# Kernel tuning notes

Measured on AMD Instinct MI355X. Metric: run time of the kernel, lower is better.

The kernel has to match this reference:

```python
import jax, jax.numpy as jnp
import numpy as np
import math

DIM = 1024
N_HEADS = 16
HEAD_DIM = DIM // N_HEADS


def rope(x):
    # x: [B, H, S, D] with D == HEAD_DIM, interleaved even/odd rotation
    S = x.shape[-2]
    D = x.shape[-1]
    pos = jnp.arange(S, dtype=x.dtype)[:, None]              # [S, 1]
    dim = jnp.arange(D // 2, dtype=x.dtype)[None, :]         # [1, D/2]
    theta = pos / jnp.exp(2.0 * dim / D * math.log(10000.0))  # [S, D/2]
    sin = jnp.sin(theta)[None, None]                          # [1,1,S,D/2]
    cos = jnp.cos(theta)[None, None]
    x1 = x[..., ::2]
    x2 = x[..., 1::2]
    out1 = x1 * cos - x2 * sin
    out2 = x1 * sin + x2 * cos
    # interleave back: stack on last axis then flatten pairs
    return jnp.stack([out1, out2], axis=-1).reshape(x.shape)


def setup_inputs() -> dict:
    key = jax.random.key(0)
    ks = jax.random.split(key, 9)
    B, S = 2, 2048
    s = 1.0 / math.sqrt(DIM)
    inp = {
        "x": jax.random.normal(ks[0], (B, S, DIM), dtype=jnp.float32),
        "wq": jax.random.normal(ks[1], (DIM, DIM), dtype=jnp.float32) * s,
        "bq": jnp.zeros((DIM,), dtype=jnp.float32),
        "wk": jax.random.normal(ks[2], (DIM, DIM), dtype=jnp.float32) * s,
        "bk": jnp.zeros((DIM,), dtype=jnp.float32),
        "wv": jax.random.normal(ks[3], (DIM, DIM), dtype=jnp.float32) * s,
        "bv": jnp.zeros((DIM,), dtype=jnp.float32),
        "wo": jax.random.normal(ks[4], (DIM, DIM), dtype=jnp.float32) * s,
        "bo": jnp.zeros((DIM,), dtype=jnp.float32),
    }
    return inp


def reference(x, wq, bq, wk, bk, wv, bv, wo, bo):
    B, S, _ = x.shape
    # torch Linear: y = x @ W^T + b
    def proj(w, b):
        y = jnp.einsum('bsd,ed->bse', x, w) + b
        return y.reshape(B, S, N_HEADS, HEAD_DIM).transpose(0, 2, 1, 3)  # [B,H,S,Dh]
    q = rope(proj(wq, bq))
    k = rope(proj(wk, bk))
    v = proj(wv, bv)
    score = jnp.einsum('bhqd,bhkd->bhqk', q, k) / math.sqrt(HEAD_DIM)
    causal = jnp.tril(jnp.ones((S, S), dtype=bool))
    score = jnp.where(causal[None, None], score, -jnp.inf)
    attn = jax.nn.softmax(score, axis=-1)
    out = jnp.einsum('bhqk,bhkd->bhqd', attn, v)
    out = out.transpose(0, 2, 1, 3).reshape(B, S, DIM)
    return jnp.einsum('bsd,ed->bse', out, wo) + bo
```

## Files before the change

### kernel.cpp

```cpp
#include <hip/hip_runtime.h>
#include <cstdint>
#include <cstddef>


typedef __bf16 bf16_t;
typedef __bf16 bf16x8 __attribute__((ext_vector_type(8)));
typedef __bf16 bf16x4 __attribute__((ext_vector_type(4)));
typedef float  f32x4  __attribute__((ext_vector_type(4)));

#define DEVFN __device__ __forceinline__

static constexpr int Bn  = 2;
static constexpr int S   = 2048;
static constexpr int DIM = 1024;
static constexpr int NH  = 16;
static constexpr int HD  = 64;
static constexpr int Mrows = Bn * S;

DEVFN f32x4 mfma16(bf16x8 a, bf16x8 b, f32x4 c) {
  return __builtin_amdgcn_mfma_f32_16x16x32_bf16(a, b, c, 0, 0, 0);
}

DEVFN void gl_lds16(const bf16_t* g, bf16_t* l) {
  __builtin_amdgcn_global_load_lds(
      (const __attribute__((address_space(1))) unsigned*)g,
      (__attribute__((address_space(3))) unsigned*)l, 16, 0, 0);
}

__global__ __launch_bounds__(256) void k_cvt(const float* __restrict__ in,
                                             bf16_t* __restrict__ out, int n) {
  int i = (blockIdx.x * 256 + threadIdx.x) * 4;
  if (i >= n) return;
  float4 v = *(const float4*)(in + i);
  bf16x4 o = { (bf16_t)v.x, (bf16_t)v.y, (bf16_t)v.z, (bf16_t)v.w };
  *(bf16x4*)(out + i) = o;
}

__global__ __launch_bounds__(256) void k_tab(float2* __restrict__ tab) {
  int i = blockIdx.x * 256 + threadIdx.x;
  int s = i >> 5, d = i & 31;
  float th = (float)s * expf(-(2.0f * (float)d / 64.0f) * logf(10000.0f));
  tab[i] = make_float2(cosf(th), sinf(th));
}

__global__ __launch_bounds__(256) void k_rope(bf16_t* __restrict__ X,
                                              const float2* __restrict__ tab,
                                              float scale) {
  int i = blockIdx.x * 256 + threadIdx.x;
  int row = i >> 7;
  int s = row & (S - 1);
  int dd = (i & 7) << 3;
  int p0 = dd >> 1;
  bf16x8 v = *(bf16x8*)(X + (size_t)i * 8);
  bf16x8 o;
#pragma unroll
  for (int j = 0; j < 4; ++j) {
    float x1 = (float)v[2 * j], x2 = (float)v[2 * j + 1];
    float2 cs = tab[s * 32 + p0 + j];
    o[2 * j]     = (bf16_t)((x1 * cs.x - x2 * cs.y) * scale);
    o[2 * j + 1] = (bf16_t)((x1 * cs.y + x2 * cs.x) * scale);
  }
  *(bf16x8*)(X + (size_t)i * 8) = o;
}

__global__ __launch_bounds__(256) void k_trans(const bf16_t* __restrict__ Vin,
                                               bf16_t* __restrict__ VT) {
  __shared__ __align__(16) bf16_t tile[64][72];
  int s0 = blockIdx.x * 64, bh = blockIdx.y;
  int b = bh >> 4, h = bh & 15;
  int t = threadIdx.x;
#pragma unroll
  for (int it = 0; it < 2; ++it) {
    int sl = (t >> 3) + it * 32, d0 = (t & 7) << 3;
    *(bf16x8*)&tile[sl][d0] =
        *(const bf16x8*)(Vin + (size_t)(b * S + s0 + sl) * DIM + h * HD + d0);
  }
  __syncthreads();
  int d = t >> 2, c0 = (t & 3) * 16;
  bf16_t buf[16];
#pragma unroll
  for (int j = 0; j < 16; ++j) buf[j] = tile[c0 + j][d];
  bf16_t* op = VT + ((size_t)bh * HD + d) * S + s0 + c0;
  *(bf16x8*)op = *(bf16x8*)&buf[0];
  *(bf16x8*)(op + 8) = *(bf16x8*)&buf[8];
}

template <bool OUTF32>
__global__ __launch_bounds__(256) void k_gemm(
    const bf16_t* __restrict__ A,
    const bf16_t* __restrict__ B0, const bf16_t* __restrict__ B1,
    const bf16_t* __restrict__ B2,
    const float* __restrict__ c0, const float* __restrict__ c1,
    const float* __restrict__ c2,
    void* O0, void* O1, void* O2, int Mg, int Ng, int Kg) {
  const bf16_t* Bw = blockIdx.z == 0 ? B0 : (blockIdx.z == 1 ? B1 : B2);
  const float* bias = blockIdx.z == 0 ? c0 : (blockIdx.z == 1 ? c1 : c2);
  void* Ov = blockIdx.z == 0 ? O0 : (blockIdx.z == 1 ? O1 : O2);

  __shared__ __align__(16) bf16_t Al[128 * 32];
  __shared__ __align__(16) bf16_t Bl[128 * 32];
  const int t = threadIdx.x, w = t >> 6, l = t & 63;
  const int lr = l & 15, lc = l >> 4;
  const int m0 = blockIdx.y * 128, n0 = blockIdx.x * 128;
  const int wr = w >> 1, wc = w & 1;
  f32x4 acc[4][4] = {};

  for (int k0 = 0; k0 < Kg; k0 += 32) {
    __syncthreads();
#pragma unroll
    for (int ld = 0; ld < 2; ++ld) {
      int c = t + ld * 256;
      int row = c >> 2, j = (c & 3) << 3;
      bf16_t* dstA = Al + (size_t)(w * 64 + ld * 256) * 8;
      bf16_t* dstB = Bl + (size_t)(w * 64 + ld * 256) * 8;
      gl_lds16(A + (size_t)(m0 + row) * Kg + k0 + j, dstA);
      gl_lds16(Bw + (size_t)(n0 + row) * Kg + k0 + j, dstB);
    }
    __syncthreads();
    bf16x8 af[4], bfr[4];
#pragma unroll
    for (int mi = 0; mi < 4; ++mi)
      af[mi] = *(const bf16x8*)(Al + (wr * 64 + mi * 16 + lr) * 32 + lc * 8);
#pragma unroll
    for (int ni = 0; ni < 4; ++ni)
      bfr[ni] = *(const bf16x8*)(Bl + (wc * 64 + ni * 16 + lr) * 32 + lc * 8);
#pragma unroll
    for (int mi = 0; mi < 4; ++mi)
#pragma unroll
      for (int ni = 0; ni < 4; ++ni)
        acc[mi][ni] = mfma16(af[mi], bfr[ni], acc[mi][ni]);
  }

#pragma unroll
  for (int ni = 0; ni < 4; ++ni) {
    int col = n0 + wc * 64 + ni * 16 + lr;
    float bv = bias[col];
#pragma unroll
    for (int mi = 0; mi < 4; ++mi) {
#pragma unroll
      for (int r = 0; r < 4; ++r) {
        int row = m0 + wr * 64 + mi * 16 + lc * 4 + r;
        float v = acc[mi][ni][r] + bv;
        if (OUTF32)
          ((float*)Ov)[(size_t)row * Ng + col] = v;
        else
          ((bf16_t*)Ov)[(size_t)row * Ng + col] = (bf16_t)v;
      }
    }
  }
}

DEVFN void stage_kv(const bf16_t* __restrict__ Kc,
                    const bf16_t* __restrict__ VT, bf16_t* Kb, bf16_t* Vb,
                    int b, int bh, int h, int k0, int t, int w) {
#pragma unroll
  for (int ld = 0; ld < 2; ++ld) {
    int c = t + ld * 256;
    int row = c >> 3;
    int j = ((c & 7) ^ (row & 7)) << 3;
    bf16_t* dstK = Kb + (size_t)(w * 64 + ld * 256) * 8;
    bf16_t* dstV = Vb + (size_t)(w * 64 + ld * 256) * 8;
    gl_lds16(Kc + (size_t)(b * S + k0 + row) * DIM + h * HD + j, dstK);
    gl_lds16(VT + ((size_t)bh * HD + row) * S + k0 + j, dstV);
  }
}

__global__ __launch_bounds__(256) void k_attn(const bf16_t* __restrict__ Q,
                                              const bf16_t* __restrict__ Kc,
                                              const bf16_t* __restrict__ VT,
                                              bf16_t* __restrict__ O) {
  __shared__ __align__(16) bf16_t Kl[2][64 * 64];
  __shared__ __align__(16) bf16_t Vl[2][64 * 64];
  __shared__ __align__(16) bf16_t Pl[4][16 * 64];
  const int t = threadIdx.x, w = t >> 6, l = t & 63;
  const int lr = l & 15, lc = l >> 4;
  const int lid = blockIdx.x + (blockIdx.y << 4);
  const int xcd = lid & 7, slot = lid >> 3;
  const int bh = xcd * 4 + (slot >> 4);
  const int a = slot & 15;
  const int b = bh >> 4, h = bh & 15;
  char* Pw = (char*)&Pl[w][0];

#pragma unroll 1
  for (int pi = 0; pi < 2; ++pi) {
    const int tile = (pi == 0) ? a : 31 - a;
    const int q0 = tile * 64;
    const int nt = tile + 1;

    bf16x8 qf[2];
    {
      const bf16_t* qp =
          Q + (size_t)(b * S + q0 + w * 16 + lr) * DIM + h * HD + lc * 8;
      qf[0] = *(const bf16x8*)qp;
      qf[1] = *(const bf16x8*)(qp + 32);
    }
    f32x4 o[4] = {};
    float m_run = -INFINITY;
    float rowsum = 0.f;

    stage_kv(Kc, VT, &Kl[0][0], &Vl[0][0], b, bh, h, 0, t, w);
    asm volatile("s_waitcnt vmcnt(0)" ::: "memory");
    __builtin_amdgcn_s_barrier();
    __builtin_amdgcn_sched_barrier(0);

#pragma unroll 1
    for (int it = 0; it < nt; ++it) {
      const int cur = it & 1;
      const bf16_t* Kb = &Kl[cur][0];
      const bf16_t* Vb = &Vl[cur][0];
      if (it + 1 < nt) {
        stage_kv(Kc, VT, &Kl[cur ^ 1][0], &Vl[cur ^ 1][0], b, bh, h,
                 (it + 1) * 64, t, w);
        asm volatile("s_waitcnt vmcnt(4)" ::: "memory");
      } else {
        asm volatile("s_waitcnt vmcnt(0)" ::: "memory");
      }
      __builtin_amdgcn_s_barrier();
      __builtin_amdgcn_sched_barrier(0);

      f32x4 s[4] = {};
      __builtin_amdgcn_s_setprio(1);
#pragma unroll
      for (int ks = 0; ks < 2; ++ks) {
#pragma unroll
        for (int ni = 0; ni < 4; ++ni) {
          int row = ni * 16 + lr;
          int off = (ks * 64 + lc * 16) ^ ((row & 7) << 4);
          bf16x8 kf = *(const bf16x8*)((const char*)Kb + row * 128 + off);
          s[ni] = mfma16(kf, qf[ks], s[ni]);
        }
      }
      __builtin_amdgcn_s_setprio(0);

      if (it == tile) {
        const int qloc = w * 16 + lr;
#pragma unroll
        for (int ni = 0; ni < 4; ++ni)
#pragma unroll
          for (int r = 0; r < 4; ++r)
            if (ni * 16 + lc * 4 + r > qloc) s[ni][r] = -INFINITY;
      }

      float pm = s[0][0];
#pragma unroll
      for (int ni = 0; ni < 4; ++ni)
#pragma unroll
        for (int r = 0; r < 4; ++r) pm = fmaxf(pm, s[ni][r]);
      pm = fmaxf(pm, __shfl_xor(pm, 16));
      pm = fmaxf(pm, __shfl_xor(pm, 32));

      if (__ballot(pm > m_run + 8.f)) {
        float mn = fmaxf(m_run, pm);
        float alpha = __expf(m_run - mn);
        m_run = mn;
        rowsum *= alpha;
#pragma unroll
        for (int r = 0; r < 4; ++r) {
          float aq = __shfl(alpha, lc * 4 + r);
#pragma unroll
          for (int ni = 0; ni < 4; ++ni) o[ni][r] *= aq;
        }
      }

      float rs = 0.f;
#pragma unroll
      for (int ni = 0; ni < 4; ++ni) {
        float p0 = __expf(s[ni][0] - m_run);
        float p1 = __expf(s[ni][1] - m_run);
        float p2 = __expf(s[ni][2] - m_run);
        float p3 = __expf(s[ni][3] - m_run);
        rs += (p0 + p1) + (p2 + p3);
        bf16x4 pb = { (bf16_t)p0, (bf16_t)p1, (bf16_t)p2, (bf16_t)p3 };
        *(bf16x4*)(Pw + (lr * 128 + ((ni * 32 + lc * 8) ^ ((lr & 7) << 4)))) =
            pb;
      }
      rs += __shfl_xor(rs, 16);
      rs += __shfl_xor(rs, 32);
      rowsum += rs;

      __builtin_amdgcn_s_setprio(1);
#pragma unroll
      for (int ks = 0; ks < 2; ++ks) {
        int off = ks * 64 + lc * 16;
        bf16x8 pa =
            *(const bf16x8*)(Pw + lr * 128 + (off ^ ((lr & 7) << 4)));
#pragma unroll
        for (int ni = 0; ni < 4; ++ni) {
          int vrow = ni * 16 + lr;
          bf16x8 vb = *(const bf16x8*)((const char*)Vb + vrow * 128 +
                                       (off ^ ((vrow & 7) << 4)));
          o[ni] = mfma16(pa, vb, o[ni]);
        }
      }
      __builtin_amdgcn_s_setprio(0);

      __builtin_amdgcn_s_barrier();
    }

    float inv[4];
#pragma unroll
    for (int r = 0; r < 4; ++r) inv[r] = 1.0f / __shfl(rowsum, lc * 4 + r);
#pragma unroll
    for (int ni = 0; ni < 4; ++ni)
#pragma unroll
      for (int r = 0; r < 4; ++r) {
        int qr = q0 + w * 16 + lc * 4 + r;
        float v = o[ni][r] * inv[r];
        O[(size_t)(b * S + qr) * DIM + h * HD + ni * 16 + lr] = (bf16_t)v;
      }
  }
}

extern "C" void kernel_launch(void* const* d_in, const int* in_sizes, int n_in,
                              void* d_out, int out_size, void* d_ws,
                              size_t ws_size, hipStream_t stream) {
  const float* x  = (const float*)d_in[0];
  const float* wq = (const float*)d_in[1];
  const float* bq = (const float*)d_in[2];
  const float* wk = (const float*)d_in[3];
  const float* bk = (const float*)d_in[4];
  const float* wv = (const float*)d_in[5];
  const float* bv = (const float*)d_in[6];
  const float* wo = (const float*)d_in[7];
  const float* bo = (const float*)d_in[8];

  const size_t MD = (size_t)Mrows * DIM;
  const size_t WD = (size_t)DIM * DIM;
  bf16_t* W = (bf16_t*)d_ws;
  bf16_t* x_bf  = W;
  bf16_t* wq_bf = x_bf + MD;
  bf16_t* wk_bf = wq_bf + WD;
  bf16_t* wv_bf = wk_bf + WD;
  bf16_t* wo_bf = wv_bf + WD;
  bf16_t* q_lin = wo_bf + WD;
  bf16_t* k_lin = q_lin + MD;
  bf16_t* v_lin = k_lin + MD;
  bf16_t* vT    = v_lin + MD;
  float2* tab   = (float2*)(vT + MD);
  bf16_t* attn_out = v_lin;

  k_cvt<<<4096, 256, 0, stream>>>(x, x_bf, (int)MD);
  k_cvt<<<1024, 256, 0, stream>>>(wq, wq_bf, (int)WD);
  k_cvt<<<1024, 256, 0, stream>>>(wk, wk_bf, (int)WD);
  k_cvt<<<1024, 256, 0, stream>>>(wv, wv_bf, (int)WD);
  k_cvt<<<1024, 256, 0, stream>>>(wo, wo_bf, (int)WD);
  k_tab<<<256, 256, 0, stream>>>(tab);

  k_gemm<false><<<dim3(DIM / 128, Mrows / 128, 3), 256, 0, stream>>>(
      x_bf, wq_bf, wk_bf, wv_bf, bq, bk, bv, q_lin, k_lin, v_lin, Mrows, DIM,
      DIM);

  k_rope<<<2048, 256, 0, stream>>>(q_lin, tab, 0.125f);
  k_rope<<<2048, 256, 0, stream>>>(k_lin, tab, 1.0f);
  k_trans<<<dim3(S / 64, Bn * NH), 256, 0, stream>>>(v_lin, vT);

  k_attn<<<dim3(16, Bn * NH), 256, 0, stream>>>(q_lin, k_lin, vT, attn_out);

  k_gemm<true><<<dim3(DIM / 128, Mrows / 128, 1), 256, 0, stream>>>(
      attn_out, wo_bf, wo_bf, wo_bf, bo, bo, bo, d_out, d_out, d_out, Mrows,
      DIM, DIM);
}
```

Before: 143.1 us.

## Fuse prep kernels, fold RoPE and V transpose into QKV GEMM, pipeline attention

The six conversion and table kernels are merged into a single prep launch. RoPE (with the query scale) and the V transpose are moved into the QKV GEMM epilogue, which removes three separate passes over Q, K and V in global memory. The attention loop is software-pipelined: QK^T for the next tile is computed before the softmax of the current one, and V uses a triple buffer. The costs are a scattered transposed-store epilogue for V, extra shuffles and table reads in the RoPE epilogue, and higher register and LDS use in attention.

```diff
diff --git a/kernel.cpp b/kernel.cpp
--- a/kernel.cpp
+++ b/kernel.cpp
@@ -27,75 +27,48 @@
       (__attribute__((address_space(3))) unsigned*)l, 16, 0, 0);
 }
 
-__global__ __launch_bounds__(256) void k_cvt(const float* __restrict__ in,
-                                             bf16_t* __restrict__ out, int n) {
-  int i = (blockIdx.x * 256 + threadIdx.x) * 4;
-  if (i >= n) return;
-  float4 v = *(const float4*)(in + i);
-  bf16x4 o = { (bf16_t)v.x, (bf16_t)v.y, (bf16_t)v.z, (bf16_t)v.w };
-  *(bf16x4*)(out + i) = o;
-}
-
-__global__ __launch_bounds__(256) void k_tab(float2* __restrict__ tab) {
-  int i = blockIdx.x * 256 + threadIdx.x;
-  int s = i >> 5, d = i & 31;
-  float th = (float)s * expf(-(2.0f * (float)d / 64.0f) * logf(10000.0f));
-  tab[i] = make_float2(cosf(th), sinf(th));
-}
-
-__global__ __launch_bounds__(256) void k_rope(bf16_t* __restrict__ X,
-                                              const float2* __restrict__ tab,
-                                              float scale) {
-  int i = blockIdx.x * 256 + threadIdx.x;
-  int row = i >> 7;
-  int s = row & (S - 1);
-  int dd = (i & 7) << 3;
-  int p0 = dd >> 1;
-  bf16x8 v = *(bf16x8*)(X + (size_t)i * 8);
-  bf16x8 o;
-#pragma unroll
-  for (int j = 0; j < 4; ++j) {
-    float x1 = (float)v[2 * j], x2 = (float)v[2 * j + 1];
-    float2 cs = tab[s * 32 + p0 + j];
-    o[2 * j]     = (bf16_t)((x1 * cs.x - x2 * cs.y) * scale);
-    o[2 * j + 1] = (bf16_t)((x1 * cs.y + x2 * cs.x) * scale);
-  }
-  *(bf16x8*)(X + (size_t)i * 8) = o;
-}
-
-__global__ __launch_bounds__(256) void k_trans(const bf16_t* __restrict__ Vin,
-                                               bf16_t* __restrict__ VT) {
-  __shared__ __align__(16) bf16_t tile[64][72];
-  int s0 = blockIdx.x * 64, bh = blockIdx.y;
-  int b = bh >> 4, h = bh & 15;
-  int t = threadIdx.x;
-#pragma unroll
-  for (int it = 0; it < 2; ++it) {
-    int sl = (t >> 3) + it * 32, d0 = (t & 7) << 3;
-    *(bf16x8*)&tile[sl][d0] =
-        *(const bf16x8*)(Vin + (size_t)(b * S + s0 + sl) * DIM + h * HD + d0);
-  }
-  __syncthreads();
-  int d = t >> 2, c0 = (t & 3) * 16;
-  bf16_t buf[16];
-#pragma unroll
-  for (int j = 0; j < 16; ++j) buf[j] = tile[c0 + j][d];
-  bf16_t* op = VT + ((size_t)bh * HD + d) * S + s0 + c0;
-  *(bf16x8*)op = *(bf16x8*)&buf[0];
-  *(bf16x8*)(op + 8) = *(bf16x8*)&buf[8];
-}
-
-template <bool OUTF32>
-__global__ __launch_bounds__(256) void k_gemm(
-    const bf16_t* __restrict__ A,
-    const bf16_t* __restrict__ B0, const bf16_t* __restrict__ B1,
-    const bf16_t* __restrict__ B2,
+__global__ __launch_bounds__(256) void k_prep(
+    const float* __restrict__ x, const float* __restrict__ wq,
+    const float* __restrict__ wk, const float* __restrict__ wv,
+    const float* __restrict__ wo, bf16_t* __restrict__ xb,
+    bf16_t* __restrict__ wqb, bf16_t* __restrict__ wkb,
+    bf16_t* __restrict__ wvb, bf16_t* __restrict__ wob,
+    float2* __restrict__ tab) {
+  const int bid = blockIdx.x;
+  if (bid < 8192) {
+    const float* src;
+    bf16_t* dst;
+    size_t base;
+    if (bid < 4096) {
+      src = x; dst = xb; base = (size_t)bid << 10;
+    } else {
+      int wsel = (bid - 4096) >> 10;
+      src = wsel == 0 ? wq : wsel == 1 ? wk : wsel == 2 ? wv : wo;
+      dst = wsel == 0 ? wqb : wsel == 1 ? wkb : wsel == 2 ? wvb : wob;
+      base = (size_t)((bid - 4096) & 1023) << 10;
+    }
+    size_t i = base + (size_t)threadIdx.x * 4;
+    float4 v = *(const float4*)(src + i);
+    bf16x4 o = { (bf16_t)v.x, (bf16_t)v.y, (bf16_t)v.z, (bf16_t)v.w };
+    *(bf16x4*)(dst + i) = o;
+  } else {
+    int i = (bid - 8192) * 256 + threadIdx.x;
+    int s = i >> 5, d = i & 31;
+    float th = (float)s * expf((float)d * -0.2878231366f);
+    tab[i] = make_float2(cosf(th), sinf(th));
+  }
+}
+
+__global__ __launch_bounds__(256) void k_gemm_qkv(
+    const bf16_t* __restrict__ A, const bf16_t* __restrict__ B0,
+    const bf16_t* __restrict__ B1, const bf16_t* __restrict__ B2,
     const float* __restrict__ c0, const float* __restrict__ c1,
-    const float* __restrict__ c2,
-    void* O0, void* O1, void* O2, int Mg, int Ng, int Kg) {
-  const bf16_t* Bw = blockIdx.z == 0 ? B0 : (blockIdx.z == 1 ? B1 : B2);
-  const float* bias = blockIdx.z == 0 ? c0 : (blockIdx.z == 1 ? c1 : c2);
-  void* Ov = blockIdx.z == 0 ? O0 : (blockIdx.z == 1 ? O1 : O2);
+    const float* __restrict__ c2, bf16_t* __restrict__ Oq,
+    bf16_t* __restrict__ Ok, bf16_t* __restrict__ VTo,
+    const float2* __restrict__ tab) {
+  const int z = blockIdx.z;
+  const bf16_t* Bw = z == 0 ? B0 : (z == 1 ? B1 : B2);
+  const float* bias = z == 0 ? c0 : (z == 1 ? c1 : c2);
 
   __shared__ __align__(16) bf16_t Al[128 * 32];
   __shared__ __align__(16) bf16_t Bl[128 * 32];
@@ -105,7 +78,7 @@
   const int wr = w >> 1, wc = w & 1;
   f32x4 acc[4][4] = {};
 
-  for (int k0 = 0; k0 < Kg; k0 += 32) {
+  for (int k0 = 0; k0 < DIM; k0 += 32) {
     __syncthreads();
 #pragma unroll
     for (int ld = 0; ld < 2; ++ld) {
@@ -113,8 +86,87 @@
       int row = c >> 2, j = (c & 3) << 3;
       bf16_t* dstA = Al + (size_t)(w * 64 + ld * 256) * 8;
       bf16_t* dstB = Bl + (size_t)(w * 64 + ld * 256) * 8;
-      gl_lds16(A + (size_t)(m0 + row) * Kg + k0 + j, dstA);
-      gl_lds16(Bw + (size_t)(n0 + row) * Kg + k0 + j, dstB);
+      gl_lds16(A + (size_t)(m0 + row) * DIM + k0 + j, dstA);
+      gl_lds16(Bw + (size_t)(n0 + row) * DIM + k0 + j, dstB);
+    }
+    __syncthreads();
+    bf16x8 af[4], bfr[4];
+#pragma unroll
+    for (int mi = 0; mi < 4; ++mi)
+      af[mi] = *(const bf16x8*)(Al + (wr * 64 + mi * 16 + lr) * 32 + lc * 8);
+#pragma unroll
+    for (int ni = 0; ni < 4; ++ni)
+      bfr[ni] = *(const bf16x8*)(Bl + (wc * 64 + ni * 16 + lr) * 32 + lc * 8);
+#pragma unroll
+    for (int mi = 0; mi < 4; ++mi)
+#pragma unroll
+      for (int ni = 0; ni < 4; ++ni)
+        acc[mi][ni] = mfma16(af[mi], bfr[ni], acc[mi][ni]);
+  }
+
+  if (z == 2) {
+    const int h = (n0 >> 6) + wc;
+#pragma unroll
+    for (int ni = 0; ni < 4; ++ni) {
+      const int d = ni * 16 + lr;
+      const float bv = bias[n0 + wc * 64 + ni * 16 + lr];
+#pragma unroll
+      for (int mi = 0; mi < 4; ++mi) {
+        int rowb = m0 + wr * 64 + mi * 16 + lc * 4;
+        int bb = rowb >> 11, ss = rowb & (S - 1);
+        bf16x4 pb = { (bf16_t)(acc[mi][ni][0] + bv),
+                      (bf16_t)(acc[mi][ni][1] + bv),
+                      (bf16_t)(acc[mi][ni][2] + bv),
+                      (bf16_t)(acc[mi][ni][3] + bv) };
+        *(bf16x4*)(VTo + ((size_t)(bb * NH + h) * HD + d) * S + ss) = pb;
+      }
+    }
+  } else {
+    bf16_t* Ov = z == 0 ? Oq : Ok;
+    const float scale = z == 0 ? 0.125f : 1.0f;
+#pragma unroll
+    for (int ni = 0; ni < 4; ++ni) {
+      const int col = n0 + wc * 64 + ni * 16 + lr;
+      const float bv = bias[col];
+      const int p0 = ni * 8 + (lr >> 1);
+#pragma unroll
+      for (int mi = 0; mi < 4; ++mi) {
+#pragma unroll
+        for (int r = 0; r < 4; ++r) {
+          int row = m0 + wr * 64 + mi * 16 + lc * 4 + r;
+          float v = acc[mi][ni][r] + bv;
+          float pt = __shfl_xor(v, 1);
+          float2 cs = tab[(row & (S - 1)) * 32 + p0];
+          float out = (lr & 1) ? (pt * cs.y + v * cs.x)
+                               : (v * cs.x - pt * cs.y);
+          Ov[(size_t)row * DIM + col] = (bf16_t)(out * scale);
+        }
+      }
+    }
+  }
+}
+
+__global__ __launch_bounds__(256) void k_gemm_out(
+    const bf16_t* __restrict__ A, const bf16_t* __restrict__ Bw,
+    const float* __restrict__ bias, float* __restrict__ Ov) {
+  __shared__ __align__(16) bf16_t Al[128 * 32];
+  __shared__ __align__(16) bf16_t Bl[128 * 32];
+  const int t = threadIdx.x, w = t >> 6, l = t & 63;
+  const int lr = l & 15, lc = l >> 4;
+  const int m0 = blockIdx.y * 128, n0 = blockIdx.x * 128;
+  const int wr = w >> 1, wc = w & 1;
+  f32x4 acc[4][4] = {};
+
+  for (int k0 = 0; k0 < DIM; k0 += 32) {
+    __syncthreads();
+#pragma unroll
+    for (int ld = 0; ld < 2; ++ld) {
+      int c = t + ld * 256;
+      int row = c >> 2, j = (c & 3) << 3;
+      bf16_t* dstA = Al + (size_t)(w * 64 + ld * 256) * 8;
+      bf16_t* dstB = Bl + (size_t)(w * 64 + ld * 256) * 8;
+      gl_lds16(A + (size_t)(m0 + row) * DIM + k0 + j, dstA);
+      gl_lds16(Bw + (size_t)(n0 + row) * DIM + k0 + j, dstB);
     }
     __syncthreads();
     bf16x8 af[4], bfr[4];
@@ -136,26 +188,21 @@
     int col = n0 + wc * 64 + ni * 16 + lr;
     float bv = bias[col];
 #pragma unroll
-    for (int mi = 0; mi < 4; ++mi) {
+    for (int mi = 0; mi < 4; ++mi)
 #pragma unroll
       for (int r = 0; r < 4; ++r) {
         int row = m0 + wr * 64 + mi * 16 + lc * 4 + r;
-        float v = acc[mi][ni][r] + bv;
-        if (OUTF32)
-          ((float*)Ov)[(size_t)row * Ng + col] = v;
-        else
-          ((bf16_t*)Ov)[(size_t)row * Ng + col] = (bf16_t)v;
-      }
-    }
+        Ov[(size_t)row * DIM + col] = acc[mi][ni][r] + bv;
+      }
   }
 }
 
 DEVFN void stage_kv(const bf16_t* __restrict__ Kc,
                     const bf16_t* __restrict__ VT, bf16_t* Kb, bf16_t* Vb,
-                    int b, int bh, int h, int k0, int t, int w) {
+                    int b, int bh, int h, int k0, int tid, int w) {
 #pragma unroll
   for (int ld = 0; ld < 2; ++ld) {
-    int c = t + ld * 256;
+    int c = tid + ld * 256;
     int row = c >> 3;
     int j = ((c & 7) ^ (row & 7)) << 3;
     bf16_t* dstK = Kb + (size_t)(w * 64 + ld * 256) * 8;
@@ -170,9 +217,9 @@
                                               const bf16_t* __restrict__ VT,
                                               bf16_t* __restrict__ O) {
   __shared__ __align__(16) bf16_t Kl[2][64 * 64];
-  __shared__ __align__(16) bf16_t Vl[2][64 * 64];
+  __shared__ __align__(16) bf16_t Vl[3][64 * 64];
   __shared__ __align__(16) bf16_t Pl[4][16 * 64];
-  const int t = threadIdx.x, w = t >> 6, l = t & 63;
+  const int tid = threadIdx.x, w = tid >> 6, l = tid & 63;
   const int lr = l & 15, lc = l >> 4;
   const int lid = blockIdx.x + (blockIdx.y << 4);
   const int xcd = lid & 7, slot = lid >> 3;
@@ -195,57 +242,66 @@
       qf[1] = *(const bf16x8*)(qp + 32);
     }
     f32x4 o[4] = {};
+    f32x4 sA[4], sB[4];
     float m_run = -INFINITY;
     float rowsum = 0.f;
 
-    stage_kv(Kc, VT, &Kl[0][0], &Vl[0][0], b, bh, h, 0, t, w);
-    asm volatile("s_waitcnt vmcnt(0)" ::: "memory");
-    __builtin_amdgcn_s_barrier();
-    __builtin_amdgcn_sched_barrier(0);
-
-#pragma unroll 1
-    for (int it = 0; it < nt; ++it) {
-      const int cur = it & 1;
-      const bf16_t* Kb = &Kl[cur][0];
-      const bf16_t* Vb = &Vl[cur][0];
-      if (it + 1 < nt) {
-        stage_kv(Kc, VT, &Kl[cur ^ 1][0], &Vl[cur ^ 1][0], b, bh, h,
-                 (it + 1) * 64, t, w);
-        asm volatile("s_waitcnt vmcnt(4)" ::: "memory");
-      } else {
-        asm volatile("s_waitcnt vmcnt(0)" ::: "memory");
-      }
-      __builtin_amdgcn_s_barrier();
-      __builtin_amdgcn_sched_barrier(0);
-
-      f32x4 s[4] = {};
+    auto qkt = [&](f32x4(&sd)[4], const bf16_t* Kb) {
+#pragma unroll
+      for (int ni = 0; ni < 4; ++ni) sd[ni] = f32x4{0.f, 0.f, 0.f, 0.f};
       __builtin_amdgcn_s_setprio(1);
 #pragma unroll
-      for (int ks = 0; ks < 2; ++ks) {
+      for (int ks = 0; ks < 2; ++ks)
 #pragma unroll
         for (int ni = 0; ni < 4; ++ni) {
           int row = ni * 16 + lr;
           int off = (ks * 64 + lc * 16) ^ ((row & 7) << 4);
           bf16x8 kf = *(const bf16x8*)((const char*)Kb + row * 128 + off);
-          s[ni] = mfma16(kf, qf[ks], s[ni]);
+          sd[ni] = mfma16(kf, qf[ks], sd[ni]);
         }
-      }
       __builtin_amdgcn_s_setprio(0);
-
-      if (it == tile) {
+    };
+
+    stage_kv(Kc, VT, &Kl[0][0], &Vl[0][0], b, bh, h, 0, tid, w);
+    if (nt > 1) {
+      stage_kv(Kc, VT, &Kl[1][0], &Vl[1][0], b, bh, h, 64, tid, w);
+      asm volatile("s_waitcnt vmcnt(4)" ::: "memory");
+    } else {
+      asm volatile("s_waitcnt vmcnt(0)" ::: "memory");
+    }
+    __builtin_amdgcn_s_barrier();
+    __builtin_amdgcn_sched_barrier(0);
+    qkt(sA, &Kl[0][0]);
+    __builtin_amdgcn_s_barrier();
+
+    auto body = [&](f32x4(&scur)[4], f32x4(&snxt)[4], int t) {
+      if (t + 2 < nt)
+        stage_kv(Kc, VT, &Kl[(t + 2) & 1][0], &Vl[(t + 2) % 3][0], b, bh, h,
+                 (t + 2) * 64, tid, w);
+      if (t + 1 < nt) {
+        if (t + 2 < nt)
+          asm volatile("s_waitcnt vmcnt(4)" ::: "memory");
+        else
+          asm volatile("s_waitcnt vmcnt(0)" ::: "memory");
+        __builtin_amdgcn_s_barrier();
+        __builtin_amdgcn_sched_barrier(0);
+        qkt(snxt, &Kl[(t + 1) & 1][0]);
+      }
+
+      if (t == nt - 1) {
         const int qloc = w * 16 + lr;
 #pragma unroll
         for (int ni = 0; ni < 4; ++ni)
 #pragma unroll
           for (int r = 0; r < 4; ++r)
-            if (ni * 16 + lc * 4 + r > qloc) s[ni][r] = -INFINITY;
-      }
-
-      float pm = s[0][0];
+            if (ni * 16 + lc * 4 + r > qloc) scur[ni][r] = -INFINITY;
+      }
+
+      float pm = scur[0][0];
 #pragma unroll
       for (int ni = 0; ni < 4; ++ni)
 #pragma unroll
-        for (int r = 0; r < 4; ++r) pm = fmaxf(pm, s[ni][r]);
+        for (int r = 0; r < 4; ++r) pm = fmaxf(pm, scur[ni][r]);
       pm = fmaxf(pm, __shfl_xor(pm, 16));
       pm = fmaxf(pm, __shfl_xor(pm, 32));
 
@@ -265,10 +321,10 @@
       float rs = 0.f;
 #pragma unroll
       for (int ni = 0; ni < 4; ++ni) {
-        float p0 = __expf(s[ni][0] - m_run);
-        float p1 = __expf(s[ni][1] - m_run);
-        float p2 = __expf(s[ni][2] - m_run);
-        float p3 = __expf(s[ni][3] - m_run);
+        float p0 = __expf(scur[ni][0] - m_run);
+        float p1 = __expf(scur[ni][1] - m_run);
+        float p2 = __expf(scur[ni][2] - m_run);
+        float p3 = __expf(scur[ni][3] - m_run);
         rs += (p0 + p1) + (p2 + p3);
         bf16x4 pb = { (bf16_t)p0, (bf16_t)p1, (bf16_t)p2, (bf16_t)p3 };
         *(bf16x4*)(Pw + (lr * 128 + ((ni * 32 + lc * 8) ^ ((lr & 7) << 4)))) =
@@ -278,12 +334,12 @@
       rs += __shfl_xor(rs, 32);
       rowsum += rs;
 
+      const bf16_t* Vb = &Vl[t % 3][0];
       __builtin_amdgcn_s_setprio(1);
 #pragma unroll
       for (int ks = 0; ks < 2; ++ks) {
         int off = ks * 64 + lc * 16;
-        bf16x8 pa =
-            *(const bf16x8*)(Pw + lr * 128 + (off ^ ((lr & 7) << 4)));
+        bf16x8 pa = *(const bf16x8*)(Pw + lr * 128 + (off ^ ((lr & 7) << 4)));
 #pragma unroll
         for (int ni = 0; ni < 4; ++ni) {
           int vrow = ni * 16 + lr;
@@ -295,6 +351,14 @@
       __builtin_amdgcn_s_setprio(0);
 
       __builtin_amdgcn_s_barrier();
+    };
+
+#pragma unroll 1
+    for (int t = 0; t < nt; ++t) {
+      if (t & 1)
+        body(sB, sA, t);
+      else
+        body(sA, sB, t);
     }
 
     float inv[4];
@@ -334,29 +398,18 @@
   bf16_t* wo_bf = wv_bf + WD;
   bf16_t* q_lin = wo_bf + WD;
   bf16_t* k_lin = q_lin + MD;
-  bf16_t* v_lin = k_lin + MD;
-  bf16_t* vT    = v_lin + MD;
+  bf16_t* attn_out = k_lin + MD;
+  bf16_t* vT    = attn_out + MD;
   float2* tab   = (float2*)(vT + MD);
-  bf16_t* attn_out = v_lin;
-
-  k_cvt<<<4096, 256, 0, stream>>>(x, x_bf, (int)MD);
-  k_cvt<<<1024, 256, 0, stream>>>(wq, wq_bf, (int)WD);
-  k_cvt<<<1024, 256, 0, stream>>>(wk, wk_bf, (int)WD);
-  k_cvt<<<1024, 256, 0, stream>>>(wv, wv_bf, (int)WD);
-  k_cvt<<<1024, 256, 0, stream>>>(wo, wo_bf, (int)WD);
-  k_tab<<<256, 256, 0, stream>>>(tab);
-
-  k_gemm<false><<<dim3(DIM / 128, Mrows / 128, 3), 256, 0, stream>>>(
-      x_bf, wq_bf, wk_bf, wv_bf, bq, bk, bv, q_lin, k_lin, v_lin, Mrows, DIM,
-      DIM);
-
-  k_rope<<<2048, 256, 0, stream>>>(q_lin, tab, 0.125f);
-  k_rope<<<2048, 256, 0, stream>>>(k_lin, tab, 1.0f);
-  k_trans<<<dim3(S / 64, Bn * NH), 256, 0, stream>>>(v_lin, vT);
+
+  k_prep<<<8448, 256, 0, stream>>>(x, wq, wk, wv, wo, x_bf, wq_bf, wk_bf,
+                                   wv_bf, wo_bf, tab);
+
+  k_gemm_qkv<<<dim3(DIM / 128, Mrows / 128, 3), 256, 0, stream>>>(
+      x_bf, wq_bf, wk_bf, wv_bf, bq, bk, bv, q_lin, k_lin, vT, tab);
 
   k_attn<<<dim3(16, Bn * NH), 256, 0, stream>>>(q_lin, k_lin, vT, attn_out);
 
-  k_gemm<true><<<dim3(DIM / 128, Mrows / 128, 1), 256, 0, stream>>>(
-      attn_out, wo_bf, wo_bf, wo_bf, bo, bo, bo, d_out, d_out, d_out, Mrows,
-      DIM, DIM);
-}
+  k_gemm_out<<<dim3(DIM / 128, Mrows / 128), 256, 0, stream>>>(
+      attn_out, wo_bf, bo, (float*)d_out);
+}
```

Measured after the change: 151.9 us. 1.06x slower.
